# Kernel tuning notes

Measured on AMD Instinct MI355X. Metric: run time of the kernel, lower is better.

## Reference

```python
import jax, jax.numpy as jnp
import numpy as np

D_MODEL = 1024
N_HEADS = 16
HEAD_DIM = D_MODEL // N_HEADS
D_FF = 4096


def setup_inputs() -> dict:
    key = jax.random.key(0)
    ks = jax.random.split(key, 16)
    s = 0.02
    x = jax.random.normal(ks[0], (4, 2048, D_MODEL), dtype=jnp.float32)
    p = {
        'x': x,
        'wq': jax.random.normal(ks[1], (D_MODEL, D_MODEL), jnp.float32) * s,
        'bq': jnp.zeros((D_MODEL,), jnp.float32),
        'wk': jax.random.normal(ks[2], (D_MODEL, D_MODEL), jnp.float32) * s,
        'bk': jnp.zeros((D_MODEL,), jnp.float32),
        'wv': jax.random.normal(ks[3], (D_MODEL, D_MODEL), jnp.float32) * s,
        'bv': jnp.zeros((D_MODEL,), jnp.float32),
        'wo': jax.random.normal(ks[4], (D_MODEL, D_MODEL), jnp.float32) * s,
        'bo': jnp.zeros((D_MODEL,), jnp.float32),
        'w1': jax.random.normal(ks[5], (D_MODEL, D_FF), jnp.float32) * s,
        'b1': jnp.zeros((D_FF,), jnp.float32),
        'w2': jax.random.normal(ks[6], (D_FF, D_MODEL), jnp.float32) * s,
        'b2': jnp.zeros((D_MODEL,), jnp.float32),
        'ln1_g': jnp.ones((D_MODEL,), jnp.float32),
        'ln1_b': jnp.zeros((D_MODEL,), jnp.float32),
        'ln2_g': jnp.ones((D_MODEL,), jnp.float32),
        'ln2_b': jnp.zeros((D_MODEL,), jnp.float32),
    }
    return p


def _layernorm(x, g, b, eps=1e-5):
    mu = jnp.mean(x, axis=-1, keepdims=True)
    var = jnp.mean(jnp.square(x - mu), axis=-1, keepdims=True)
    return (x - mu) * jax.lax.rsqrt(var + eps) * g + b


def reference(x, wq, bq, wk, bk, wv, bv, wo, bo, w1, b1, w2, b2, ln1_g, ln1_b, ln2_g, ln2_b):
    B, S, D = x.shape
    normed = _layernorm(x, ln1_g, ln1_b)
    # projections -> [B, H, S, Dh]
    def split_heads(t):
        return t.reshape(B, S, N_HEADS, HEAD_DIM).transpose(0, 2, 1, 3)
    q = split_heads(normed @ wq + bq)
    k = split_heads(normed @ wk + bk)
    v = split_heads(normed @ wv + bv)
    scale = 1.0 / jnp.sqrt(jnp.float32(HEAD_DIM))
    scores = jnp.einsum('bhqd,bhkd->bhqk', q, k) * scale  # [B,H,S,S]
    causal = jnp.tril(jnp.ones((S, S), dtype=bool))
    scores = jnp.where(causal[None, None], scores, -jnp.inf)
    probs = jax.nn.softmax(scores, axis=-1)
    attn = jnp.einsum('bhqk,bhkd->bhqd', probs, v)
    attn = attn.transpose(0, 2, 1, 3).reshape(B, S, D)
    x = x + (attn @ wo + bo)
    h = _layernorm(x, ln2_g, ln2_b)
    h = jax.nn.gelu(h @ w1 + b1, approximate=False)
    x = x + (h @ w2 + b2)
    return x
```

## Files before the change

### kernel.cpp

```cpp
#include <hip/hip_runtime.h>
#include <hip/hip_bf16.h>
#include <math.h>

typedef __attribute__((ext_vector_type(8))) short short8;
typedef __attribute__((ext_vector_type(4))) float floatx4;

#define D_MODEL 1024
#define N_HEADS 16
#define HEAD_DIM 64
#define D_FF 4096
#define BATCH 4
#define SEQ 2048
#define NTOK (BATCH * SEQ)

#define GLOBAL_AS __attribute__((address_space(1)))
#define LDS_AS __attribute__((address_space(3)))

__device__ __forceinline__ void async_ld16(const void* g, void* l) {
    __builtin_amdgcn_global_load_lds((GLOBAL_AS const unsigned int*)g,
                                     (LDS_AS unsigned int*)l, 16, 0, 0);
}

__global__ void wtrans_kernel(const float* __restrict__ in, __hip_bfloat16* __restrict__ out,
                              int R, int C) {
    __shared__ float tile[32][33];
    const int c0 = blockIdx.x * 32, r0 = blockIdx.y * 32;
    const int tx = threadIdx.x & 31, ty = threadIdx.x >> 5;
#pragma unroll
    for (int i = 0; i < 4; ++i) {
        int r = ty + i * 8;
        tile[r][tx] = in[(size_t)(r0 + r) * C + c0 + tx];
    }
    __syncthreads();
#pragma unroll
    for (int i = 0; i < 4; ++i) {
        int r = ty + i * 8;
        out[(size_t)(c0 + r) * R + r0 + tx] = __float2bfloat16(tile[tx][r]);
    }
}

__global__ void bconcat_kernel(const float* __restrict__ bq, const float* __restrict__ bk,
                               const float* __restrict__ bv, float* __restrict__ out) {
    const int i = blockIdx.x * 256 + threadIdx.x;
    float v = (i < 1024) ? bq[i] : (i < 2048 ? bk[i - 1024] : bv[i - 2048]);
    out[i] = v;
}

__global__ void vtrans_kernel(const __hip_bfloat16* __restrict__ in,
                              __hip_bfloat16* __restrict__ out) {
    __shared__ short T[64 * 64];
    const int tid = threadIdx.x;
    const int bh = blockIdx.y;
    const int s0 = blockIdx.x * 64;
    const int4* src = (const int4*)(in + (size_t)bh * SEQ * 64 + (size_t)s0 * 64);
#pragma unroll
    for (int i = 0; i < 2; ++i) {
        int idx = i * 256 + tid;
        int s = idx >> 3, g = idx & 7;
        *(int4*)&T[s * 64 + ((g ^ (s & 7)) * 8)] = src[idx];
    }
    __syncthreads();
    const int dh = tid & 63;
    const int sgb = tid >> 6;
#pragma unroll
    for (int i = 0; i < 2; ++i) {
        const int sg = sgb + i * 4;
        short8 vv;
#pragma unroll
        for (int j = 0; j < 8; ++j) {
            const int s = sg * 8 + j;
            vv[j] = T[s * 64 + (((dh >> 3) ^ j) * 8) + (dh & 7)];
        }
        *(short8*)((short*)out + (size_t)bh * 64 * SEQ + (size_t)dh * SEQ + s0 + sg * 8) = vv;
    }
}

__global__ void ln_kernel(const float* __restrict__ x, const float* __restrict__ g,
                          const float* __restrict__ b, __hip_bfloat16* __restrict__ out) {
    const int row = blockIdx.x;
    const int tid = threadIdx.x;
    const float4 v = ((const float4*)(x + (size_t)row * D_MODEL))[tid];
    float s = v.x + v.y + v.z + v.w;
    float s2 = v.x * v.x + v.y * v.y + v.z * v.z + v.w * v.w;
#pragma unroll
    for (int off = 32; off >= 1; off >>= 1) {
        s += __shfl_xor(s, off, 64);
        s2 += __shfl_xor(s2, off, 64);
    }
    __shared__ float ss[4], ss2[4];
    const int wid = tid >> 6, lane = tid & 63;
    if (lane == 0) { ss[wid] = s; ss2[wid] = s2; }
    __syncthreads();
    const float tot = ss[0] + ss[1] + ss[2] + ss[3];
    const float tot2 = ss2[0] + ss2[1] + ss2[2] + ss2[3];
    const float mu = tot * (1.0f / D_MODEL);
    const float var = tot2 * (1.0f / D_MODEL) - mu * mu;
    const float rsq = rsqrtf(var + 1e-5f);
    const float vv[4] = {v.x, v.y, v.z, v.w};
#pragma unroll
    for (int j = 0; j < 4; ++j) {
        int c = tid * 4 + j;
        out[(size_t)row * D_MODEL + c] = __float2bfloat16((vv[j] - mu) * rsq * g[c] + b[c]);
    }
}

#define BM 128
#define BN 128
#define BK 64

template <int MODE>
__global__ void gemm_kernel(const __hip_bfloat16* __restrict__ A,
                            const __hip_bfloat16* __restrict__ Bt,
                            const float* __restrict__ bias,
                            const float* __restrict__ resid,
                            void* __restrict__ outp, int M, int N, int K, float scale) {
    __shared__ __hip_bfloat16 As[BM * BK];
    __shared__ __hip_bfloat16 Bs[BN * BK];
    const int tid = threadIdx.x;
    const int lane = tid & 63;
    const int w = tid >> 6;
    const int wm = w >> 1, wn = w & 1;
    const int m0 = blockIdx.x * BM;
    const int n0 = blockIdx.y * BN;

    const int srow = lane >> 3;
    const int lgrp = (lane & 7) ^ srow;

    const size_t a_base = (size_t)(m0 + w * 32 + srow) * K + lgrp * 8;
    const size_t b_base = (size_t)(n0 + w * 32 + srow) * K + lgrp * 8;

    const floatx4 vzero = {0.f, 0.f, 0.f, 0.f};
    floatx4 acc[4][4];
#pragma unroll
    for (int i = 0; i < 4; ++i)
#pragma unroll
        for (int j = 0; j < 4; ++j) acc[i][j] = vzero;

    const int lcol = lane & 15;
    const int quad = lane >> 4;
    const int arow = wm * 64 + lcol;
    const int brow = wn * 64 + lcol;
    const int l7 = lcol & 7;

    for (int kt = 0; kt < K; kt += BK) {
        __syncthreads();
#pragma unroll
        for (int j = 0; j < 4; ++j)
            async_ld16(A + a_base + kt + (size_t)(j * 8) * K, &As[(w * 32 + j * 8) * BK]);
#pragma unroll
        for (int j = 0; j < 4; ++j)
            async_ld16(Bt + b_base + kt + (size_t)(j * 8) * K, &Bs[(w * 32 + j * 8) * BK]);
        __syncthreads();
#pragma unroll
        for (int ks = 0; ks < 2; ++ks) {
            const int g = ((ks * 4 + quad) ^ l7) * 8;
            short8 af[4], bf[4];
#pragma unroll
            for (int mt = 0; mt < 4; ++mt) af[mt] = *(const short8*)&As[(arow + mt * 16) * BK + g];
#pragma unroll
            for (int nt = 0; nt < 4; ++nt) bf[nt] = *(const short8*)&Bs[(brow + nt * 16) * BK + g];
#pragma unroll
            for (int mt = 0; mt < 4; ++mt)
#pragma unroll
                for (int nt = 0; nt < 4; ++nt)
                    acc[mt][nt] = __builtin_amdgcn_mfma_f32_16x16x32_bf16(af[mt], bf[nt], acc[mt][nt], 0, 0, 0);
        }
    }

    const int lrow4 = quad * 4;
#pragma unroll
    for (int mt = 0; mt < 4; ++mt) {
#pragma unroll
        for (int nt = 0; nt < 4; ++nt) {
#pragma unroll
            for (int r = 0; r < 4; ++r) {
                const int gm = m0 + wm * 64 + mt * 16 + lrow4 + r;
                const int gn = n0 + wn * 64 + nt * 16 + lcol;
                float v = acc[mt][nt][r] + bias[gn];
                if (MODE == 0) {
                    const int which = gn >> 10;
                    const int rest = gn & 1023;
                    if (which == 0) v *= scale;
                    const int bb = gm >> 11, s = gm & (SEQ - 1);
                    const int h = rest >> 6, dh = rest & (HEAD_DIM - 1);
                    ((__hip_bfloat16*)outp)[(size_t)which * NTOK * D_MODEL +
                        ((size_t)(bb * N_HEADS + h) * SEQ + s) * HEAD_DIM + dh] =
                        __float2bfloat16(v);
                } else if (MODE == 1) {
                    v += resid[(size_t)gm * N + gn];
                    ((float*)outp)[(size_t)gm * N + gn] = v;
                } else if (MODE == 2) {
                    const float ge = 0.5f * v * (1.0f + erff(v * 0.70710678118654752f));
                    ((__hip_bfloat16*)outp)[(size_t)gm * N + gn] = __float2bfloat16(ge);
                } else {
                    v += resid[(size_t)gm * N + gn];
                    ((float*)outp)[(size_t)gm * N + gn] = v;
                }
            }
        }
    }
}

__global__ void attn_kernel(const __hip_bfloat16* __restrict__ q,
                            const __hip_bfloat16* __restrict__ k,
                            const __hip_bfloat16* __restrict__ vt,
                            __hip_bfloat16* __restrict__ o) {
    __shared__ __hip_bfloat16 Ks[2][64 * 64];
    __shared__ __hip_bfloat16 VTs[2][64 * 64];
    __shared__ __hip_bfloat16 Ps[4][32 * 72];

    const int tid = threadIdx.x;
    const int lane = tid & 63;
    const int w = tid >> 6;
    const int bh = blockIdx.y;
    const int b = bh >> 4, h = bh & 15;
    const int qt = (blockIdx.x + (blockIdx.y >> 2)) & 15;
    const int q0 = qt * 128;
    const size_t hb = (size_t)bh * SEQ * HEAD_DIM;
    const size_t vhb = (size_t)bh * HEAD_DIM * SEQ;

    const int lcol = lane & 15;
    const int quad = lane >> 4;
    const int koff = quad * 8;
    const int lrow4 = quad * 4;
    const int srow = lane >> 3;
    const int lgrp = (lane & 7) ^ srow;

    short8 aq[2][2];
#pragma unroll
    for (int rb = 0; rb < 2; ++rb)
#pragma unroll
        for (int ks = 0; ks < 2; ++ks)
            aq[rb][ks] = *(const short8*)(q + hb +
                (size_t)(q0 + w * 32 + rb * 16 + lcol) * 64 + ks * 32 + koff);

    const floatx4 vzero = {0.f, 0.f, 0.f, 0.f};
    floatx4 ao[2][4];
    floatx4 aol[2];
#pragma unroll
    for (int rb = 0; rb < 2; ++rb) {
        aol[rb] = vzero;
#pragma unroll
        for (int nt = 0; nt < 4; ++nt) ao[rb][nt] = vzero;
    }
    short8 vone;
#pragma unroll
    for (int j = 0; j < 8; ++j) vone[j] = (short)0x3F80;

    const int qmax_wave = q0 + w * 32 + 31;

    for (int kv0 = 0; kv0 < q0 + 128; kv0 += 128) {
        __syncthreads();
#pragma unroll
        for (int sub = 0; sub < 2; ++sub)
#pragma unroll
            for (int j = 0; j < 2; ++j) {
                const int rr = w * 16 + j * 8 + srow;
                async_ld16(k + hb + (size_t)(kv0 + sub * 64 + rr) * 64 + lgrp * 8,
                           &Ks[sub][(w * 16 + j * 8) * 64]);
                async_ld16(vt + vhb + (size_t)rr * SEQ + kv0 + sub * 64 + lgrp * 8,
                           &VTs[sub][(w * 16 + j * 8) * 64]);
            }
        __syncthreads();

#pragma unroll
        for (int sub = 0; sub < 2; ++sub) {
            const int kvb = kv0 + sub * 64;
            if (kvb > qmax_wave) continue;

            floatx4 sc[2][4];
#pragma unroll
            for (int rb = 0; rb < 2; ++rb)
#pragma unroll
                for (int nt = 0; nt < 4; ++nt) sc[rb][nt] = vzero;
#pragma unroll
            for (int nt = 0; nt < 4; ++nt) {
                const int krow = nt * 16 + lcol;
                const short8 bk0 = *(const short8*)&Ks[sub][krow * 64 + ((quad ^ (lcol & 7)) * 8)];
                const short8 bk1 = *(const short8*)&Ks[sub][krow * 64 + (((4 + quad) ^ (lcol & 7)) * 8)];
#pragma unroll
                for (int rb = 0; rb < 2; ++rb) {
                    sc[rb][nt] = __builtin_amdgcn_mfma_f32_16x16x32_bf16(aq[rb][0], bk0, sc[rb][nt], 0, 0, 0);
                    sc[rb][nt] = __builtin_amdgcn_mfma_f32_16x16x32_bf16(aq[rb][1], bk1, sc[rb][nt], 0, 0, 0);
                }
            }
            if (kvb + 63 > q0 + w * 32) {
#pragma unroll
                for (int rb = 0; rb < 2; ++rb)
#pragma unroll
                    for (int nt = 0; nt < 4; ++nt)
#pragma unroll
                        for (int r = 0; r < 4; ++r) {
                            const int qrow = q0 + w * 32 + rb * 16 + lrow4 + r;
                            const int kcol = kvb + nt * 16 + lcol;
                            if (kcol > qrow) sc[rb][nt][r] = -1e30f;
                        }
            }
#pragma unroll
            for (int rb = 0; rb < 2; ++rb)
#pragma unroll
                for (int nt = 0; nt < 4; ++nt)
#pragma unroll
                    for (int r = 0; r < 4; ++r)
                        Ps[w][(rb * 16 + lrow4 + r) * 72 + nt * 16 + lcol] =
                            __float2bfloat16(exp2f(sc[rb][nt][r]));
#pragma unroll
            for (int ks = 0; ks < 2; ++ks) {
                short8 vbf[4];
#pragma unroll
                for (int nt = 0; nt < 4; ++nt)
                    vbf[nt] = *(const short8*)&VTs[sub][(nt * 16 + lcol) * 64 +
                                                       ((((ks * 4) + quad) ^ (lcol & 7)) * 8)];
#pragma unroll
                for (int rb = 0; rb < 2; ++rb) {
                    const short8 pa = *(const short8*)&Ps[w][(rb * 16 + lcol) * 72 + ks * 32 + koff];
                    aol[rb] = __builtin_amdgcn_mfma_f32_16x16x32_bf16(pa, vone, aol[rb], 0, 0, 0);
#pragma unroll
                    for (int nt = 0; nt < 4; ++nt)
                        ao[rb][nt] = __builtin_amdgcn_mfma_f32_16x16x32_bf16(pa, vbf[nt], ao[rb][nt], 0, 0, 0);
                }
            }
        }
    }
#pragma unroll
    for (int rb = 0; rb < 2; ++rb)
#pragma unroll
        for (int nt = 0; nt < 4; ++nt)
#pragma unroll
            for (int r = 0; r < 4; ++r) {
                const int qrow = q0 + w * 32 + rb * 16 + lrow4 + r;
                const float ov = ao[rb][nt][r] / aol[rb][r];
                o[((size_t)(b * SEQ) + qrow) * D_MODEL + h * HEAD_DIM + nt * 16 + lcol] =
                    __float2bfloat16(ov);
            }
}

extern "C" void kernel_launch(void* const* d_in, const int* in_sizes, int n_in,
                              void* d_out, int out_size, void* d_ws, size_t ws_size,
                              hipStream_t stream) {
    (void)in_sizes; (void)n_in; (void)out_size; (void)ws_size;
    const float* x    = (const float*)d_in[0];
    const float* wq   = (const float*)d_in[1];
    const float* bq   = (const float*)d_in[2];
    const float* wk   = (const float*)d_in[3];
    const float* bk   = (const float*)d_in[4];
    const float* wv   = (const float*)d_in[5];
    const float* bv   = (const float*)d_in[6];
    const float* wo   = (const float*)d_in[7];
    const float* bo   = (const float*)d_in[8];
    const float* w1   = (const float*)d_in[9];
    const float* b1   = (const float*)d_in[10];
    const float* w2   = (const float*)d_in[11];
    const float* b2   = (const float*)d_in[12];
    const float* ln1g = (const float*)d_in[13];
    const float* ln1b = (const float*)d_in[14];
    const float* ln2g = (const float*)d_in[15];
    const float* ln2b = (const float*)d_in[16];
    float* out = (float*)d_out;

    char* ws = (char*)d_ws;
    size_t off = 0;
    auto alloc = [&](size_t bytes) { void* p = ws + off; off += bytes; return p; };
    __hip_bfloat16* wqkvT = (__hip_bfloat16*)alloc((size_t)3072 * 1024 * 2);
    __hip_bfloat16* woT = (__hip_bfloat16*)alloc((size_t)1024 * 1024 * 2);
    __hip_bfloat16* w1T = (__hip_bfloat16*)alloc((size_t)4096 * 1024 * 2);
    __hip_bfloat16* w2T = (__hip_bfloat16*)alloc((size_t)4096 * 1024 * 2);
    float* bqkv = (float*)alloc((size_t)3072 * 4);
    __hip_bfloat16* normed = (__hip_bfloat16*)alloc((size_t)NTOK * D_MODEL * 2);
    __hip_bfloat16* qb = (__hip_bfloat16*)alloc((size_t)NTOK * D_MODEL * 2);
    __hip_bfloat16* kb = (__hip_bfloat16*)alloc((size_t)NTOK * D_MODEL * 2);
    __hip_bfloat16* vb = (__hip_bfloat16*)alloc((size_t)NTOK * D_MODEL * 2);
    __hip_bfloat16* attnb = (__hip_bfloat16*)alloc((size_t)NTOK * D_MODEL * 2);
    float* x1 = (float*)alloc((size_t)NTOK * D_MODEL * 4);
    __hip_bfloat16* hh = (__hip_bfloat16*)alloc((size_t)NTOK * D_FF * 2);
    __hip_bfloat16* vtb = (__hip_bfloat16*)hh;

    const float QSCALE = 0.125f * 1.44269504088896f;

    const dim3 blk(256);
    wtrans_kernel<<<dim3(32, 32), blk, 0, stream>>>(wq, wqkvT, 1024, 1024);
    wtrans_kernel<<<dim3(32, 32), blk, 0, stream>>>(wk, wqkvT + (size_t)1024 * 1024, 1024, 1024);
    wtrans_kernel<<<dim3(32, 32), blk, 0, stream>>>(wv, wqkvT + (size_t)2048 * 1024, 1024, 1024);
    wtrans_kernel<<<dim3(32, 32), blk, 0, stream>>>(wo, woT, 1024, 1024);
    wtrans_kernel<<<dim3(128, 32), blk, 0, stream>>>(w1, w1T, 1024, 4096);
    wtrans_kernel<<<dim3(32, 128), blk, 0, stream>>>(w2, w2T, 4096, 1024);
    bconcat_kernel<<<dim3(12), blk, 0, stream>>>(bq, bk, bv, bqkv);

    ln_kernel<<<NTOK, blk, 0, stream>>>(x, ln1g, ln1b, normed);

    gemm_kernel<0><<<dim3(NTOK / BM, 3072 / BN), blk, 0, stream>>>(normed, wqkvT, bqkv, nullptr, qb, NTOK, 3072, 1024, QSCALE);

    vtrans_kernel<<<dim3(SEQ / 64, BATCH * N_HEADS), blk, 0, stream>>>(vb, vtb);

    attn_kernel<<<dim3(SEQ / 128, BATCH * N_HEADS), blk, 0, stream>>>(qb, kb, vtb, attnb);

    gemm_kernel<1><<<dim3(NTOK / BM, 1024 / BN), blk, 0, stream>>>(attnb, woT, bo, x, x1, NTOK, 1024, 1024, 1.0f);

    ln_kernel<<<NTOK, blk, 0, stream>>>(x1, ln2g, ln2b, normed);

    gemm_kernel<2><<<dim3(NTOK / BM, D_FF / BN), blk, 0, stream>>>(normed, w1T, b1, nullptr, hh, NTOK, D_FF, 1024, 1.0f);
    gemm_kernel<3><<<dim3(NTOK / BM, 1024 / BN), blk, 0, stream>>>(hh, w2T, b2, x1, out, NTOK, 1024, D_FF, 1.0f);
}
```

Measured before the change: 544.7 us.

## Fuse V transpose into QKV GEMM epilogue and pair causal query tiles

The QKV GEMM epilogue now writes V directly in transposed [bh, dh, seq] layout with packed 4-element stores, so the separate vtrans kernel and the V buffer are removed. The attention kernel processes two query tiles per block (tile i and 15-i) so every block does the same amount of causal work, and the grid is halved. It also computes S transposed (K as the A operand), writes P with packed swizzled stores, and adds launch bounds. The cost is more registers per thread for the doubled accumulators, which may limit occupancy.

```diff
diff --git a/kernel.cpp b/kernel.cpp
--- a/kernel.cpp
+++ b/kernel.cpp
@@ -3,6 +3,7 @@
 #include <math.h>
 
 typedef __attribute__((ext_vector_type(8))) short short8;
+typedef __attribute__((ext_vector_type(4))) short short4v;
 typedef __attribute__((ext_vector_type(4))) float floatx4;
 
 #define D_MODEL 1024
@@ -21,6 +22,11 @@
                                      (LDS_AS unsigned int*)l, 16, 0, 0);
 }
 
+__device__ __forceinline__ short bf16s(float v) {
+    __hip_bfloat16 h = __float2bfloat16(v);
+    return *(short*)&h;
+}
+
 __global__ void wtrans_kernel(const float* __restrict__ in, __hip_bfloat16* __restrict__ out,
                               int R, int C) {
     __shared__ float tile[32][33];
@@ -44,35 +50,6 @@
     const int i = blockIdx.x * 256 + threadIdx.x;
     float v = (i < 1024) ? bq[i] : (i < 2048 ? bk[i - 1024] : bv[i - 2048]);
     out[i] = v;
-}
-
-__global__ void vtrans_kernel(const __hip_bfloat16* __restrict__ in,
-                              __hip_bfloat16* __restrict__ out) {
-    __shared__ short T[64 * 64];
-    const int tid = threadIdx.x;
-    const int bh = blockIdx.y;
-    const int s0 = blockIdx.x * 64;
-    const int4* src = (const int4*)(in + (size_t)bh * SEQ * 64 + (size_t)s0 * 64);
-#pragma unroll
-    for (int i = 0; i < 2; ++i) {
-        int idx = i * 256 + tid;
-        int s = idx >> 3, g = idx & 7;
-        *(int4*)&T[s * 64 + ((g ^ (s & 7)) * 8)] = src[idx];
-    }
-    __syncthreads();
-    const int dh = tid & 63;
-    const int sgb = tid >> 6;
-#pragma unroll
-    for (int i = 0; i < 2; ++i) {
-        const int sg = sgb + i * 4;
-        short8 vv;
-#pragma unroll
-        for (int j = 0; j < 8; ++j) {
-            const int s = sg * 8 + j;
-            vv[j] = T[s * 64 + (((dh >> 3) ^ j) * 8) + (dh & 7)];
-        }
-        *(short8*)((short*)out + (size_t)bh * 64 * SEQ + (size_t)dh * SEQ + s0 + sg * 8) = vv;
-    }
 }
 
 __global__ void ln_kernel(const float* __restrict__ x, const float* __restrict__ g,
@@ -113,7 +90,8 @@
                             const __hip_bfloat16* __restrict__ Bt,
                             const float* __restrict__ bias,
                             const float* __restrict__ resid,
-                            void* __restrict__ outp, int M, int N, int K, float scale) {
+                            void* __restrict__ outp, __hip_bfloat16* __restrict__ vtout,
+                            int M, int N, int K, float scale) {
     __shared__ __hip_bfloat16 As[BM * BK];
     __shared__ __hip_bfloat16 Bs[BN * BK];
     const int tid = threadIdx.x;
@@ -172,84 +150,101 @@
     for (int mt = 0; mt < 4; ++mt) {
 #pragma unroll
         for (int nt = 0; nt < 4; ++nt) {
-#pragma unroll
-            for (int r = 0; r < 4; ++r) {
-                const int gm = m0 + wm * 64 + mt * 16 + lrow4 + r;
-                const int gn = n0 + wn * 64 + nt * 16 + lcol;
-                float v = acc[mt][nt][r] + bias[gn];
-                if (MODE == 0) {
-                    const int which = gn >> 10;
-                    const int rest = gn & 1023;
-                    if (which == 0) v *= scale;
-                    const int bb = gm >> 11, s = gm & (SEQ - 1);
-                    const int h = rest >> 6, dh = rest & (HEAD_DIM - 1);
-                    ((__hip_bfloat16*)outp)[(size_t)which * NTOK * D_MODEL +
-                        ((size_t)(bb * N_HEADS + h) * SEQ + s) * HEAD_DIM + dh] =
-                        __float2bfloat16(v);
-                } else if (MODE == 1) {
-                    v += resid[(size_t)gm * N + gn];
-                    ((float*)outp)[(size_t)gm * N + gn] = v;
-                } else if (MODE == 2) {
-                    const float ge = 0.5f * v * (1.0f + erff(v * 0.70710678118654752f));
-                    ((__hip_bfloat16*)outp)[(size_t)gm * N + gn] = __float2bfloat16(ge);
+            const int gm0 = m0 + wm * 64 + mt * 16 + lrow4;
+            const int gn = n0 + wn * 64 + nt * 16 + lcol;
+            const float bb_ = bias[gn];
+            if (MODE == 0) {
+                const int which = gn >> 10;
+                const int rest = gn & 1023;
+                const int bb = gm0 >> 11, s = gm0 & (SEQ - 1);
+                const int h = rest >> 6, dh = rest & (HEAD_DIM - 1);
+                if (which == 2) {
+                    short4v pk;
+#pragma unroll
+                    for (int r = 0; r < 4; ++r) pk[r] = bf16s(acc[mt][nt][r] + bb_);
+                    *(short4v*)(vtout + ((size_t)((bb * N_HEADS + h) * HEAD_DIM + dh)) * SEQ + s) = pk;
                 } else {
-                    v += resid[(size_t)gm * N + gn];
-                    ((float*)outp)[(size_t)gm * N + gn] = v;
+                    const float sc = (which == 0) ? scale : 1.0f;
+#pragma unroll
+                    for (int r = 0; r < 4; ++r) {
+                        float v = (acc[mt][nt][r] + bb_) * sc;
+                        ((__hip_bfloat16*)outp)[(size_t)which * NTOK * D_MODEL +
+                            ((size_t)(bb * N_HEADS + h) * SEQ + s + r) * HEAD_DIM + dh] =
+                            __float2bfloat16(v);
+                    }
+                }
+            } else {
+#pragma unroll
+                for (int r = 0; r < 4; ++r) {
+                    const int gm = gm0 + r;
+                    float v = acc[mt][nt][r] + bb_;
+                    if (MODE == 1 || MODE == 3) {
+                        v += resid[(size_t)gm * N + gn];
+                        ((float*)outp)[(size_t)gm * N + gn] = v;
+                    } else {
+                        const float ge = 0.5f * v * (1.0f + erff(v * 0.70710678118654752f));
+                        ((__hip_bfloat16*)outp)[(size_t)gm * N + gn] = __float2bfloat16(ge);
+                    }
                 }
             }
         }
     }
 }
 
-__global__ void attn_kernel(const __hip_bfloat16* __restrict__ q,
-                            const __hip_bfloat16* __restrict__ k,
-                            const __hip_bfloat16* __restrict__ vt,
-                            __hip_bfloat16* __restrict__ o) {
+__global__ void __launch_bounds__(256, 2)
+attn_kernel(const __hip_bfloat16* __restrict__ q,
+            const __hip_bfloat16* __restrict__ k,
+            const __hip_bfloat16* __restrict__ vt,
+            __hip_bfloat16* __restrict__ o) {
     __shared__ __hip_bfloat16 Ks[2][64 * 64];
     __shared__ __hip_bfloat16 VTs[2][64 * 64];
-    __shared__ __hip_bfloat16 Ps[4][32 * 72];
+    __shared__ __hip_bfloat16 Ps[4][2][32 * 64];
 
     const int tid = threadIdx.x;
     const int lane = tid & 63;
     const int w = tid >> 6;
     const int bh = blockIdx.y;
     const int b = bh >> 4, h = bh & 15;
-    const int qt = (blockIdx.x + (blockIdx.y >> 2)) & 15;
-    const int q0 = qt * 128;
+    const int q0t[2] = {(int)blockIdx.x * 128, (15 - (int)blockIdx.x) * 128};
     const size_t hb = (size_t)bh * SEQ * HEAD_DIM;
     const size_t vhb = (size_t)bh * HEAD_DIM * SEQ;
 
     const int lcol = lane & 15;
     const int quad = lane >> 4;
-    const int koff = quad * 8;
+    const int l7 = lcol & 7;
     const int lrow4 = quad * 4;
     const int srow = lane >> 3;
     const int lgrp = (lane & 7) ^ srow;
 
-    short8 aq[2][2];
-#pragma unroll
-    for (int rb = 0; rb < 2; ++rb)
-#pragma unroll
-        for (int ks = 0; ks < 2; ++ks)
-            aq[rb][ks] = *(const short8*)(q + hb +
-                (size_t)(q0 + w * 32 + rb * 16 + lcol) * 64 + ks * 32 + koff);
+    short8 aq[2][2][2];
+#pragma unroll
+    for (int t = 0; t < 2; ++t)
+#pragma unroll
+        for (int rb = 0; rb < 2; ++rb)
+#pragma unroll
+            for (int ks = 0; ks < 2; ++ks)
+                aq[t][rb][ks] = *(const short8*)(q + hb +
+                    (size_t)(q0t[t] + w * 32 + rb * 16 + lcol) * 64 + ks * 32 + quad * 8);
 
     const floatx4 vzero = {0.f, 0.f, 0.f, 0.f};
-    floatx4 ao[2][4];
-    floatx4 aol[2];
-#pragma unroll
-    for (int rb = 0; rb < 2; ++rb) {
-        aol[rb] = vzero;
-#pragma unroll
-        for (int nt = 0; nt < 4; ++nt) ao[rb][nt] = vzero;
-    }
+    floatx4 ao[2][2][4];
+    floatx4 aol[2][2];
+#pragma unroll
+    for (int t = 0; t < 2; ++t)
+#pragma unroll
+        for (int rb = 0; rb < 2; ++rb) {
+            aol[t][rb] = vzero;
+#pragma unroll
+            for (int nt = 0; nt < 4; ++nt) ao[t][rb][nt] = vzero;
+        }
     short8 vone;
 #pragma unroll
     for (int j = 0; j < 8; ++j) vone[j] = (short)0x3F80;
 
-    const int qmax_wave = q0 + w * 32 + 31;
-
-    for (int kv0 = 0; kv0 < q0 + 128; kv0 += 128) {
+    const int rounds = 16 - blockIdx.x;
+
+    for (int rd = 0; rd < rounds; ++rd) {
+        const int kv0 = rd * 128;
         __syncthreads();
 #pragma unroll
         for (int sub = 0; sub < 2; ++sub)
@@ -266,73 +261,79 @@
 #pragma unroll
         for (int sub = 0; sub < 2; ++sub) {
             const int kvb = kv0 + sub * 64;
-            if (kvb > qmax_wave) continue;
-
-            floatx4 sc[2][4];
-#pragma unroll
-            for (int rb = 0; rb < 2; ++rb)
-#pragma unroll
-                for (int nt = 0; nt < 4; ++nt) sc[rb][nt] = vzero;
-#pragma unroll
-            for (int nt = 0; nt < 4; ++nt) {
-                const int krow = nt * 16 + lcol;
-                const short8 bk0 = *(const short8*)&Ks[sub][krow * 64 + ((quad ^ (lcol & 7)) * 8)];
-                const short8 bk1 = *(const short8*)&Ks[sub][krow * 64 + (((4 + quad) ^ (lcol & 7)) * 8)];
+#pragma unroll
+            for (int t = 0; t < 2; ++t) {
+                const int qw0 = q0t[t] + w * 32;
+                if (kvb > qw0 + 31) continue;
+
+                floatx4 st[2][4];
+#pragma unroll
+                for (int rb = 0; rb < 2; ++rb)
+#pragma unroll
+                    for (int ntk = 0; ntk < 4; ++ntk) st[rb][ntk] = vzero;
+#pragma unroll
+                for (int ntk = 0; ntk < 4; ++ntk) {
+                    const int krow = ntk * 16 + lcol;
+                    const short8 ka0 = *(const short8*)&Ks[sub][krow * 64 + ((quad ^ l7) * 8)];
+                    const short8 ka1 = *(const short8*)&Ks[sub][krow * 64 + (((4 + quad) ^ l7) * 8)];
+#pragma unroll
+                    for (int rb = 0; rb < 2; ++rb) {
+                        st[rb][ntk] = __builtin_amdgcn_mfma_f32_16x16x32_bf16(ka0, aq[t][rb][0], st[rb][ntk], 0, 0, 0);
+                        st[rb][ntk] = __builtin_amdgcn_mfma_f32_16x16x32_bf16(ka1, aq[t][rb][1], st[rb][ntk], 0, 0, 0);
+                    }
+                }
+                const bool diag = (kvb + 63 > qw0);
 #pragma unroll
                 for (int rb = 0; rb < 2; ++rb) {
-                    sc[rb][nt] = __builtin_amdgcn_mfma_f32_16x16x32_bf16(aq[rb][0], bk0, sc[rb][nt], 0, 0, 0);
-                    sc[rb][nt] = __builtin_amdgcn_mfma_f32_16x16x32_bf16(aq[rb][1], bk1, sc[rb][nt], 0, 0, 0);
-                }
-            }
-            if (kvb + 63 > q0 + w * 32) {
-#pragma unroll
-                for (int rb = 0; rb < 2; ++rb)
-#pragma unroll
-                    for (int nt = 0; nt < 4; ++nt)
+                    const int qrow = qw0 + rb * 16 + lcol;
+#pragma unroll
+                    for (int ntk = 0; ntk < 4; ++ntk) {
+                        short4v pk;
 #pragma unroll
                         for (int r = 0; r < 4; ++r) {
-                            const int qrow = q0 + w * 32 + rb * 16 + lrow4 + r;
-                            const int kcol = kvb + nt * 16 + lcol;
-                            if (kcol > qrow) sc[rb][nt][r] = -1e30f;
+                            const int kcol = kvb + ntk * 16 + lrow4 + r;
+                            float p = exp2f(st[rb][ntk][r]);
+                            if (diag && kcol > qrow) p = 0.f;
+                            pk[r] = bf16s(p);
                         }
-            }
-#pragma unroll
-            for (int rb = 0; rb < 2; ++rb)
-#pragma unroll
-                for (int nt = 0; nt < 4; ++nt)
-#pragma unroll
-                    for (int r = 0; r < 4; ++r)
-                        Ps[w][(rb * 16 + lrow4 + r) * 72 + nt * 16 + lcol] =
-                            __float2bfloat16(exp2f(sc[rb][nt][r]));
-#pragma unroll
-            for (int ks = 0; ks < 2; ++ks) {
-                short8 vbf[4];
-#pragma unroll
-                for (int nt = 0; nt < 4; ++nt)
-                    vbf[nt] = *(const short8*)&VTs[sub][(nt * 16 + lcol) * 64 +
-                                                       ((((ks * 4) + quad) ^ (lcol & 7)) * 8)];
-#pragma unroll
-                for (int rb = 0; rb < 2; ++rb) {
-                    const short8 pa = *(const short8*)&Ps[w][(rb * 16 + lcol) * 72 + ks * 32 + koff];
-                    aol[rb] = __builtin_amdgcn_mfma_f32_16x16x32_bf16(pa, vone, aol[rb], 0, 0, 0);
-#pragma unroll
-                    for (int nt = 0; nt < 4; ++nt)
-                        ao[rb][nt] = __builtin_amdgcn_mfma_f32_16x16x32_bf16(pa, vbf[nt], ao[rb][nt], 0, 0, 0);
+                        const int grp = ntk * 2 + (quad >> 1);
+                        *(short4v*)&Ps[w][t][(rb * 16 + lcol) * 64 +
+                                            ((grp ^ l7) * 8) + (quad & 1) * 4] = pk;
+                    }
+                }
+#pragma unroll
+                for (int ks = 0; ks < 2; ++ks) {
+                    short8 vbf[4];
+#pragma unroll
+                    for (int ntv = 0; ntv < 4; ++ntv)
+                        vbf[ntv] = *(const short8*)&VTs[sub][(ntv * 16 + lcol) * 64 +
+                                                            (((ks * 4 + quad) ^ l7) * 8)];
+#pragma unroll
+                    for (int rb = 0; rb < 2; ++rb) {
+                        const short8 pa = *(const short8*)&Ps[w][t][(rb * 16 + lcol) * 64 +
+                                                                   (((ks * 4 + quad) ^ l7) * 8)];
+                        aol[t][rb] = __builtin_amdgcn_mfma_f32_16x16x32_bf16(pa, vone, aol[t][rb], 0, 0, 0);
+#pragma unroll
+                        for (int ntv = 0; ntv < 4; ++ntv)
+                            ao[t][rb][ntv] = __builtin_amdgcn_mfma_f32_16x16x32_bf16(pa, vbf[ntv], ao[t][rb][ntv], 0, 0, 0);
+                    }
                 }
             }
         }
     }
 #pragma unroll
-    for (int rb = 0; rb < 2; ++rb)
-#pragma unroll
-        for (int nt = 0; nt < 4; ++nt)
-#pragma unroll
-            for (int r = 0; r < 4; ++r) {
-                const int qrow = q0 + w * 32 + rb * 16 + lrow4 + r;
-                const float ov = ao[rb][nt][r] / aol[rb][r];
-                o[((size_t)(b * SEQ) + qrow) * D_MODEL + h * HEAD_DIM + nt * 16 + lcol] =
-                    __float2bfloat16(ov);
-            }
+    for (int t = 0; t < 2; ++t)
+#pragma unroll
+        for (int rb = 0; rb < 2; ++rb)
+#pragma unroll
+            for (int ntv = 0; ntv < 4; ++ntv)
+#pragma unroll
+                for (int r = 0; r < 4; ++r) {
+                    const int qrow = q0t[t] + w * 32 + rb * 16 + lrow4 + r;
+                    const float ov = ao[t][rb][ntv][r] / aol[t][rb][r];
+                    o[((size_t)(b * SEQ) + qrow) * D_MODEL + h * HEAD_DIM + ntv * 16 + lcol] =
+                        __float2bfloat16(ov);
+                }
 }
 
 extern "C" void kernel_launch(void* const* d_in, const int* in_sizes, int n_in,
@@ -369,7 +370,6 @@
     __hip_bfloat16* normed = (__hip_bfloat16*)alloc((size_t)NTOK * D_MODEL * 2);
     __hip_bfloat16* qb = (__hip_bfloat16*)alloc((size_t)NTOK * D_MODEL * 2);
     __hip_bfloat16* kb = (__hip_bfloat16*)alloc((size_t)NTOK * D_MODEL * 2);
-    __hip_bfloat16* vb = (__hip_bfloat16*)alloc((size_t)NTOK * D_MODEL * 2);
     __hip_bfloat16* attnb = (__hip_bfloat16*)alloc((size_t)NTOK * D_MODEL * 2);
     float* x1 = (float*)alloc((size_t)NTOK * D_MODEL * 4);
     __hip_bfloat16* hh = (__hip_bfloat16*)alloc((size_t)NTOK * D_FF * 2);
@@ -388,16 +388,14 @@
 
     ln_kernel<<<NTOK, blk, 0, stream>>>(x, ln1g, ln1b, normed);
 
-    gemm_kernel<0><<<dim3(NTOK / BM, 3072 / BN), blk, 0, stream>>>(normed, wqkvT, bqkv, nullptr, qb, NTOK, 3072, 1024, QSCALE);
-
-    vtrans_kernel<<<dim3(SEQ / 64, BATCH * N_HEADS), blk, 0, stream>>>(vb, vtb);
-
-    attn_kernel<<<dim3(SEQ / 128, BATCH * N_HEADS), blk, 0, stream>>>(qb, kb, vtb, attnb);
-
-    gemm_kernel<1><<<dim3(NTOK / BM, 1024 / BN), blk, 0, stream>>>(attnb, woT, bo, x, x1, NTOK, 1024, 1024, 1.0f);
+    gemm_kernel<0><<<dim3(NTOK / BM, 3072 / BN), blk, 0, stream>>>(normed, wqkvT, bqkv, nullptr, qb, vtb, NTOK, 3072, 1024, QSCALE);
+
+    attn_kernel<<<dim3(8, BATCH * N_HEADS), blk, 0, stream>>>(qb, kb, vtb, attnb);
+
+    gemm_kernel<1><<<dim3(NTOK / BM, 1024 / BN), blk, 0, stream>>>(attnb, woT, bo, x, x1, nullptr, NTOK, 1024, 1024, 1.0f);
 
     ln_kernel<<<NTOK, blk, 0, stream>>>(x1, ln2g, ln2b, normed);
 
-    gemm_kernel<2><<<dim3(NTOK / BM, D_FF / BN), blk, 0, stream>>>(normed, w1T, b1, nullptr, hh, NTOK, D_FF, 1024, 1.0f);
-    gemm_kernel<3><<<dim3(NTOK / BM, 1024 / BN), blk, 0, stream>>>(hh, w2T, b2, x1, out, NTOK, 1024, D_FF, 1.0f);
-}
+    gemm_kernel<2><<<dim3(NTOK / BM, D_FF / BN), blk, 0, stream>>>(normed, w1T, b1, nullptr, hh, nullptr, NTOK, D_FF, 1024, 1.0f);
+    gemm_kernel<3><<<dim3(NTOK / BM, 1024 / BN), blk, 0, stream>>>(hh, w2T, b2, x1, out, nullptr, NTOK, 1024, D_FF, 1.0f);
+}
```

After: 514.3 us. -5.6%, faster.
